# Performance work log

Measured on AMD Instinct MI355X. Metric: run time of the kernel, lower is better.

## Reference

```python
import jax, jax.numpy as jnp
import numpy as np
import math

# Static config (matches init_kwargs): C4 rotation group, 14x14 grid
B = 2
CIN = 96
MID = 96
HEADS = 8
COUT = 96
G = 4            # group elements (0/90/180/270 deg rotations)
S = 14           # spatial size == max_pos_embedding
HID = 16         # hidden width of the row/col embedding MLP (Conv2d 1->16)
DPOS = MID // 3                  # 32: row / col embedding dims
DG = MID - 2 * DPOS              # 32: group embedding dim


def setup_inputs() -> dict:
    key = jax.random.key(0)
    ks = jax.random.split(key, 12)

    def lin(k, shape, scale):
        return jax.random.normal(k, shape, jnp.float32) * scale

    x = jax.random.normal(ks[0], (B, CIN, G, S, S), jnp.float32)
    # 1x1x1 Conv3d weights == per-position linear layers [out, in]
    Wq = lin(ks[1], (MID * HEADS, CIN), 1.0 / np.sqrt(CIN)); bq = jnp.zeros((MID * HEADS,), jnp.float32)
    Wk = lin(ks[2], (MID * HEADS, CIN), 1.0 / np.sqrt(CIN)); bk = jnp.zeros((MID * HEADS,), jnp.float32)
    Wv = lin(ks[3], (MID * HEADS, CIN), 1.0 / np.sqrt(CIN)); bv = jnp.zeros((MID * HEADS,), jnp.float32)
    Wo = lin(ks[4], (COUT, MID * HEADS), 1.0 / np.sqrt(MID * HEADS)); bo = jnp.zeros((COUT,), jnp.float32)
    # row embedding MLP: scalar -> 16 -> LayerNorm -> Swish -> DPOS
    rw1 = lin(ks[5], (HID,), 1.0); rb1 = jnp.zeros((HID,), jnp.float32)
    rgam = jnp.ones((HID,), jnp.float32); rbet = jnp.zeros((HID,), jnp.float32)
    rw2 = lin(ks[6], (HID, DPOS), 1.0 / np.sqrt(HID)); rb2 = jnp.zeros((DPOS,), jnp.float32)
    # col embedding MLP
    cw1 = lin(ks[7], (HID,), 1.0); cb1 = jnp.zeros((HID,), jnp.float32)
    cgam = jnp.ones((HID,), jnp.float32); cbet = jnp.zeros((HID,), jnp.float32)
    cw2 = lin(ks[8], (HID, DPOS), 1.0 / np.sqrt(HID)); cb2 = jnp.zeros((DPOS,), jnp.float32)
    # group element embedding table
    gemb = lin(ks[9], (G, DG), 0.02)

    # Relative-position buffers: rel coordinate (k-i)/(S-1) in [-1,1], rotated by
    # each group element (left action of the rotation on R^2).  [G, S, S, S, S]
    d = (jnp.arange(S)[None, :] - jnp.arange(S)[:, None]).astype(jnp.float32) / (S - 1)
    dr = jnp.broadcast_to(d[:, None, :, None], (S, S, S, S))   # row offset (k-i)
    dc = jnp.broadcast_to(d[None, :, None, :], (S, S, S, S))   # col offset (l-j)
    ang = jnp.arange(G, dtype=jnp.float32) * (np.pi / 2.0)
    cs = jnp.cos(ang)[:, None, None, None, None]
    sn = jnp.sin(ang)[:, None, None, None, None]
    row_rel = cs * dr - sn * dc
    col_rel = sn * dr + cs * dc
    # relative group-element indices acted on by each group element v: [G, G, G]
    gi = jnp.arange(G)
    g_idx = (gi[None, None, :] - gi[None, :, None] + gi[:, None, None]) % G

    return {"x": x, "Wq": Wq, "bq": bq, "Wk": Wk, "bk": bk, "Wv": Wv, "bv": bv,
            "Wo": Wo, "bo": bo,
            "rw1": rw1, "rb1": rb1, "rgam": rgam, "rbet": rbet, "rw2": rw2, "rb2": rb2,
            "cw1": cw1, "cb1": cb1, "cgam": cgam, "cbet": cbet, "cw2": cw2, "cb2": cb2,
            "gemb": gemb, "row_rel": row_rel, "col_rel": col_rel, "g_idx": g_idx}


def _embed(rel, w1, b1, gam, bet, w2, b2):
    # Conv2d(1->16, k=1) + channel LayerNorm + Swish + Conv2d(16->DPOS, k=1)
    h = rel[..., None] * w1 + b1                                   # [..., 16]
    mu = jnp.mean(h, axis=-1, keepdims=True)
    var = jnp.var(h, axis=-1, keepdims=True)
    h = (h - mu) / jnp.sqrt(var + 1e-5) * gam + bet
    h = h * jax.nn.sigmoid(h)                                      # Swish
    return h @ w2 + b2                                             # [..., DPOS]


def reference(x, Wq, bq, Wk, bk, Wv, bv, Wo, bo,
              rw1, rb1, rgam, rbet, rw2, rb2,
              cw1, cb1, cgam, cbet, cw2, cb2,
              gemb, row_rel, col_rel, g_idx):
    b = x.shape[0]

    def proj(W, bias):
        y = jnp.einsum('bcgij,dc->bdgij', x, W) + bias[None, :, None, None, None]
        return y.reshape(b, MID, HEADS, G, S, S)   # split channels as (mid, heads)

    q = proj(Wq, bq)
    k = proj(Wk, bk)
    v = proj(Wv, bv)

    q_row = q[:, :DPOS]
    q_col = q[:, DPOS:2 * DPOS]
    q_grp = q[:, 2 * DPOS:]

    row_e = _embed(row_rel, rw1, rb1, rgam, rbet, rw2, rb2)        # [G,S,S,S,S,DPOS]
    col_e = _embed(col_rel, cw1, cb1, cgam, cbet, cw2, cb2)

    row_s = jnp.einsum('bchgij,vijklc->bhvgijkl', q_row, row_e)
    col_s = jnp.einsum('bchgij,vijklc->bhvgijkl', q_col, col_e)
    g_s = jnp.einsum('bchgij,vgmc->bhvgijm', q_grp, gemb[g_idx])
    content = jnp.einsum('bchgij,bchmkl->bhgijmkl', q, k)

    # broadcast add into [b, h, v, g, i, j, m, k, l]
    scores = (jnp.expand_dims(row_s + col_s, -3)
              + g_s[..., None, None]
              + content[:, :, None]) / math.sqrt(CIN)

    sh = scores.shape
    probs = jax.nn.softmax(scores.reshape(sh[:-3] + (-1,)), axis=-1).reshape(sh)

    vo = jnp.einsum('bhvgijmkl,bchmkl->bchvij', probs, v)
    vo = vo.reshape(b, MID * HEADS, G, S, S)
    return jnp.einsum('bcgij,dc->bdgij', vo, Wo) + bo[None, :, None, None, None]
```

## Files before the change

### kernel.cpp

```cpp
#include <hip/hip_runtime.h>
#include <hip/hip_bf16.h>

constexpr int kB   = 2;
constexpr int kH   = 8;
constexpr int kG   = 4;
constexpr int kS   = 14;
constexpr int kSS  = 196;
constexpr int kKey = 784;
constexpr int kKeyP = 800;
constexpr int kMid = 96;
constexpr int kQR  = 28;
constexpr int kPS  = 808;
constexpr int kTS  = 36;
constexpr float kScl = 0.10206207261596577f;
constexpr float kK2  = 0.14724663682f;
constexpr float kCc  = 11.5415603272f;

typedef __attribute__((ext_vector_type(8))) short bf16x8;
typedef __attribute__((ext_vector_type(4))) float f32x4;

constexpr size_t SZ_QKb = (size_t)kB*kH*kG*kSS*kMid/2;
constexpr size_t OFF_Qb = 0;
constexpr size_t OFF_Kb = OFF_Qb + SZ_QKb;
constexpr size_t OFF_V  = OFF_Kb + SZ_QKb;
constexpr size_t SZ_V   = (size_t)kB*kH*kMid*kKeyP/2;
constexpr size_t OFF_FR = OFF_V + SZ_V;
constexpr size_t OFF_FC = OFF_FR + 27*32;
constexpr size_t OFF_WOH = OFF_FC + 27*32;

__global__ __launch_bounds__(256)
void k_qkv(const float* __restrict__ x,
           const float* __restrict__ Wq, const float* __restrict__ bq,
           const float* __restrict__ Wk, const float* __restrict__ bk,
           const float* __restrict__ Wv, const float* __restrict__ bv,
           __hip_bfloat16* __restrict__ Qb, __hip_bfloat16* __restrict__ Kb,
           __hip_bfloat16* __restrict__ Vb,
           const float* __restrict__ rw1, const float* __restrict__ rb1,
           const float* __restrict__ rgam, const float* __restrict__ rbet,
           const float* __restrict__ rw2, const float* __restrict__ rb2,
           const float* __restrict__ cw1, const float* __restrict__ cb1,
           const float* __restrict__ cgam, const float* __restrict__ cbet,
           const float* __restrict__ cw2, const float* __restrict__ cb2,
           float* __restrict__ frow, float* __restrict__ fcol,
           const float* __restrict__ Wo, __hip_bfloat16* __restrict__ Woh,
           float* __restrict__ out0) {
  const int bid = blockIdx.x;
  const int ten = blockIdx.y;
  const int i = bid % 14;
  const int g = (bid / 14) % 4;
  const int b = bid / 56;
  const float* W    = (ten == 0) ? Wq : (ten == 1) ? Wk : Wv;
  const float* bias = (ten == 0) ? bq : (ten == 1) ? bk : bv;

  {
    int zidx = (ten*112 + bid)*256 + threadIdx.x;
    if (zidx < 37632) ((float4*)out0)[zidx] = make_float4(0.f, 0.f, 0.f, 0.f);
  }

  __shared__ alignas(16) float xs[14][100];
  for (int idx = threadIdx.x; idx < 96*14; idx += 256) {
    int cin = idx / 14, j = idx % 14;
    xs[j][cin] = x[((size_t)(b*96 + cin)*4 + g)*196 + i*14 + j];
  }
  __syncthreads();

  for (int d = threadIdx.x; d < 768; d += 256) {
    int c = d >> 3, h = d & 7;
    float bvv = bias[d];
    float acc[14];
#pragma unroll
    for (int j = 0; j < 14; ++j) acc[j] = bvv;
    const float* wrow = W + (size_t)d * 96;
    for (int cc = 0; cc < 96; cc += 4) {
      float4 w = *(const float4*)(wrow + cc);
#pragma unroll
      for (int j = 0; j < 14; ++j) {
        float4 xv = *(const float4*)(&xs[j][cc]);
        acc[j] += w.x*xv.x + w.y*xv.y + w.z*xv.z + w.w*xv.w;
      }
    }
    if (ten == 2) {
      __hip_bfloat16* op = Vb + ((size_t)((b*8 + h)*96 + c))*kKeyP + (i*14)*4 + g;
#pragma unroll
      for (int j = 0; j < 14; ++j) op[j*4] = __float2bfloat16(acc[j]);
    } else {
      __hip_bfloat16* dst = (ten == 0) ? Qb : Kb;
      __hip_bfloat16* op = dst + ((size_t)((b*8 + h)*4 + g)*196 + i*14)*96 + c;
#pragma unroll
      for (int j = 0; j < 14; ++j) op[(size_t)j*96] = __float2bfloat16(acc[j]);
    }
  }

  if (ten == 1) {
    for (int idx = bid*256 + threadIdx.x; idx < 73728; idx += 112*256) {
      int h = idx / 9216, rem = idx - h*9216;
      int d = rem / 96, c = rem - d*96;
      Woh[idx] = __float2bfloat16(Wo[(size_t)d*768 + c*8 + h]);
    }
  }
  if (ten == 2 && bid < 16) {
    for (int idx = threadIdx.x; idx < 96*16; idx += 256) {
      int c = idx >> 4, kp = idx & 15;
      Vb[((size_t)(bid*96 + c))*kKeyP + kKey + kp] = __float2bfloat16(0.f);
    }
  }
  if (ten == 0 && bid == 0 && threadIdx.x < 54) {
    int t = threadIdx.x;
    int which = t / 27;
    int n = t % 27;
    float tv = (float)(n - 13) / 13.0f;
    const float* w1  = which ? cw1  : rw1;
    const float* b1  = which ? cb1  : rb1;
    const float* gam = which ? cgam : rgam;
    const float* bet = which ? cbet : rbet;
    const float* w2  = which ? cw2  : rw2;
    const float* b2  = which ? cb2  : rb2;
    float h[16];
    float mu = 0.f;
#pragma unroll
    for (int d = 0; d < 16; ++d) { h[d] = tv * w1[d] + b1[d]; mu += h[d]; }
    mu *= (1.0f/16.0f);
    float var = 0.f;
#pragma unroll
    for (int d = 0; d < 16; ++d) { float z = h[d] - mu; var += z*z; }
    var *= (1.0f/16.0f);
    float rstd = rsqrtf(var + 1e-5f);
#pragma unroll
    for (int d = 0; d < 16; ++d) {
      float z = (h[d] - mu) * rstd * gam[d] + bet[d];
      h[d] = z / (1.0f + expf(-z));
    }
    float* outp = (which ? fcol : frow) + n*32;
    for (int c = 0; c < 32; ++c) {
      float o = b2[c];
#pragma unroll
      for (int d = 0; d < 16; ++d) o += h[d] * w2[d*32 + c];
      outp[c] = o;
    }
  }
}

__global__ __launch_bounds__(512, 4)
void k_attn(const __hip_bfloat16* __restrict__ Qb, const __hip_bfloat16* __restrict__ Kb,
            const float* __restrict__ frow_g, const float* __restrict__ fcol_g,
            const float* __restrict__ gemb_g,
            const __hip_bfloat16* __restrict__ Vb,
            const __hip_bfloat16* __restrict__ Woh,
            const float* __restrict__ bo, float* __restrict__ out) {
  const int tid = threadIdx.x;
  const int bid = blockIdx.x;
  const int jhalf = bid & 1;
  const int t2 = bid >> 1;
  const int qi = t2 % 14;
  const int hh = (t2 / 14) % 8;
  const int bb = t2 / 112;
  const int bh = bb*8 + hh;

  __shared__ alignas(16) char poolA[19104];
  __shared__ alignas(16) __hip_bfloat16 contl[kQR][kPS];
  __shared__ alignas(16) float ArrE[kQR][28];
  __shared__ alignas(16) float AclE[kQR][28];
  __shared__ alignas(16) float AgEall[4][kQR][4];
  __shared__ float T[4][kQR][14];
  __shared__ float DinvS[4][kQR];

  float (*qs)[96] = (float(*)[96])poolA;
  float* frowS = (float*)(poolA + 10752);
  float* fcolS = (float*)(poolA + 10752 + 3888);
  float* gembS = (float*)(poolA + 10752 + 2*3888);
  __hip_bfloat16 (*vos)[104] = (__hip_bfloat16(*)[104])poolA;

  const short* Qs = (const short*)Qb;
  const short* Ks = (const short*)Kb;

  for (int idx = tid; idx < kQR*96; idx += 512) {
    int q = idx / 96, c = idx - q*96;
    int g = q / 7, jq = q - g*7;
    qs[q][c] = __bfloat162float(
        Qb[((size_t)((bh*4 + g)*kSS + qi*14 + jhalf*7 + jq))*96 + c]);
  }
  for (int idx = tid; idx < 864; idx += 512) {
    int s = idx >> 5, c = idx & 31;
    frowS[s*kTS + c] = frow_g[idx] * kK2;
    fcolS[s*kTS + c] = fcol_g[idx] * kK2;
  }
  if (tid < 128) gembS[(tid >> 5)*kTS + (tid & 31)] = gemb_g[tid] * kK2;
  __syncthreads();

  for (int idx = tid; idx < kQR*24; idx += 512) {
    int r = idx / 24, c2 = idx - r*24;
    contl[r][784 + c2] = __float2bfloat16(0.f);
  }
  {
    const int lane = tid & 63;
    const int wave = tid >> 6;
    const int col  = lane & 15;
    const int quad = lane >> 4;

    bf16x8 afrag[2][3];
#pragma unroll
    for (int mt = 0; mt < 2; ++mt) {
      int m = mt*16 + col;
      int q = (m < kQR) ? m : 0;
      const short* qrow = Qs +
          ((size_t)((bh*4 + q/7)*kSS + qi*14 + jhalf*7 + q%7))*96;
#pragma unroll
      for (int ks = 0; ks < 3; ++ks)
        afrag[mt][ks] = *(const bf16x8*)(qrow + ks*32 + quad*8);
    }

    for (int nt = wave; nt < 49; nt += 8) {
      int kl = nt*16 + col;
      const short* krow = Ks + ((size_t)(bh*kKey + kl))*96;
      bf16x8 b0 = *(const bf16x8*)(krow + 0*32 + quad*8);
      bf16x8 b1 = *(const bf16x8*)(krow + 1*32 + quad*8);
      bf16x8 b2 = *(const bf16x8*)(krow + 2*32 + quad*8);
      f32x4 c0 = {0.f,0.f,0.f,0.f};
      f32x4 c1 = {0.f,0.f,0.f,0.f};
      c0 = __builtin_amdgcn_mfma_f32_16x16x32_bf16(afrag[0][0], b0, c0, 0, 0, 0);
      c0 = __builtin_amdgcn_mfma_f32_16x16x32_bf16(afrag[0][1], b1, c0, 0, 0, 0);
      c0 = __builtin_amdgcn_mfma_f32_16x16x32_bf16(afrag[0][2], b2, c0, 0, 0, 0);
      c1 = __builtin_amdgcn_mfma_f32_16x16x32_bf16(afrag[1][0], b0, c1, 0, 0, 0);
      c1 = __builtin_amdgcn_mfma_f32_16x16x32_bf16(afrag[1][1], b1, c1, 0, 0, 0);
      c1 = __builtin_amdgcn_mfma_f32_16x16x32_bf16(afrag[1][2], b2, c1, 0, 0, 0);
      int ijn = kl % 196, mk = kl / 196;
#pragma unroll
      for (int r = 0; r < 4; ++r) {
        int q0 = quad*4 + r;
        contl[q0][ijn*4 + mk] = __float2bfloat16(exp2f(c0[r]*kK2 - kCc));
        int q1 = 16 + quad*4 + r;
        if (q1 < kQR)
          contl[q1][ijn*4 + mk] = __float2bfloat16(exp2f(c1[r]*kK2 - kCc));
      }
    }
  }

  for (int t = tid; t < kQR*58; t += 512) {
    int q = t / 58, s = t - q*58;
    float acc = 0.f;
    if (s < 27) {
#pragma unroll
      for (int c = 0; c < 32; ++c) acc += qs[q][c] * frowS[s*kTS + c];
      ArrE[q][s] = exp2f(acc);
    } else if (s < 54) {
      int n = s - 27;
#pragma unroll
      for (int c = 0; c < 32; ++c) acc += qs[q][32+c] * fcolS[n*kTS + c];
      AclE[q][n] = exp2f(acc);
    } else {
      int p = s - 54;
#pragma unroll
      for (int c = 0; c < 32; ++c) acc += qs[q][64+c] * gembS[p*kTS + c];
      float e = exp2f(acc);
      int gq = q / 7;
#pragma unroll
      for (int vv = 0; vv < 4; ++vv)
        AgEall[vv][q][(p + gq - vv + 8) & 3] = e;
    }
  }
  __syncthreads();

  const int actv = (tid < 392);
  const int qB  = actv ? (tid / 14) : 0;
  const int kkB = actv ? (tid % 14) : 0;
  const int jlB = jhalf*7 + (qB % 7);
  const int daB = kkB - qi;
  const int half = actv ? (tid / 196) : 0;
  const int ijC  = actv ? (tid % 196) : 0;
  const int kkC = ijC / 14;
  const int llC = ijC % 14;
  const int daC = kkC - qi;

  if (actv) {
    f32x4 ag0 = *(const f32x4*)(&AgEall[0][qB][0]);
    f32x4 ag1 = *(const f32x4*)(&AgEall[1][qB][0]);
    f32x4 ag2 = *(const f32x4*)(&AgEall[2][qB][0]);
    f32x4 ag3 = *(const f32x4*)(&AgEall[3][qB][0]);
    const float* Ar = &ArrE[qB][13];
    const float* Ac = &AclE[qB][13];
    float a0 = 0.f, a1 = 0.f, a2 = 0.f, a3 = 0.f;
#pragma unroll
    for (int ll = 0; ll < 14; ++ll) {
      const int db = ll - jlB;
      ushort4 u = *(const ushort4*)(&contl[qB][(kkB*14 + ll)*4]);
      float e0 = __uint_as_float((unsigned)u.x << 16);
      float e1 = __uint_as_float((unsigned)u.y << 16);
      float e2 = __uint_as_float((unsigned)u.z << 16);
      float e3 = __uint_as_float((unsigned)u.w << 16);
      a0 += Ac[ db] * (e0*ag0.x + e1*ag0.y + e2*ag0.z + e3*ag0.w);
      a1 += Ar[-db] * (e0*ag1.x + e1*ag1.y + e2*ag1.z + e3*ag1.w);
      a2 += Ac[-db] * (e0*ag2.x + e1*ag2.y + e2*ag2.z + e3*ag2.w);
      a3 += Ar[ db] * (e0*ag3.x + e1*ag3.y + e2*ag3.z + e3*ag3.w);
    }
    T[0][qB][kkB] = Ar[ daB] * a0;
    T[1][qB][kkB] = Ac[ daB] * a1;
    T[2][qB][kkB] = Ar[-daB] * a2;
    T[3][qB][kkB] = Ac[-daB] * a3;
  }
  __syncthreads();
  if (tid < 112) {
    int v = tid / 28, q = tid - v*28;
    float dsum = 0.f;
#pragma unroll
    for (int kk = 0; kk < 14; ++kk) dsum += T[v][q][kk];
    DinvS[v][q] = 1.0f / dsum;
  }
  __syncthreads();

  if (actv) {
    unsigned p32[kQR];
#pragma unroll
    for (int q = 0; q < kQR; ++q)
      p32[q] = *(const unsigned*)(&contl[q][ijC*4 + half*2]);
#pragma unroll
    for (int v = 0; v < 4; ++v) {
      const int s1a = (v==0) ? 1 : (v==2) ? -1 : 0;
      const int s1b = (v==1) ? -1 : (v==3) ? 1 : 0;
      const int s2a = (v==1) ? 1 : (v==3) ? -1 : 0;
      const int s2b = (v==0) ? 1 : (v==2) ? -1 : 0;
#pragma unroll
      for (int jq = 0; jq < 7; ++jq) {
        const int db = llC - (jhalf*7 + jq);
        const int ai = s1a*daC + s1b*db, ci = s2a*daC + s2b*db;
        float am0 = 0.f, am1 = 0.f;
#pragma unroll
        for (int gq = 0; gq < 4; ++gq) {
          const int q = gq*7 + jq;
          const float fq = ArrE[q][13 + ai] * AclE[q][13 + ci] * DinvS[v][q];
          unsigned u = p32[q];
          float e0 = __uint_as_float(u << 16);
          float e1 = __uint_as_float(u & 0xffff0000u);
          am0 += e0 * (AgEall[v][q][half*2]     * fq);
          am1 += e1 * (AgEall[v][q][half*2 + 1] * fq);
        }
        __hip_bfloat16* pp = &contl[jq*4 + v][ijC*4 + half*2];
        pp[0] = __float2bfloat16(am0);
        pp[1] = __float2bfloat16(am1);
      }
    }
  }
  __syncthreads();

  const int lane = tid & 63;
  const int wave = tid >> 6;
  const int col  = lane & 15;
  const int quad = lane >> 4;
  const int b_ = bh >> 3, h_ = bh & 7;

  {
    const short* Bp = (const short*)Vb + ((size_t)bh*96)*kKeyP + quad*8;
#pragma unroll
    for (int tk = 0; tk < 2; ++tk) {
      int t = wave + tk*8;
      if (t < 12) {
        int mt = t / 6, nt = t - mt*6;
        int crow = nt*16 + col;
        int prow = mt*16 + col; if (prow >= kQR) prow = 0;
        const short* ap = (const short*)(&contl[prow][0]) + quad*8;
        const short* bp = Bp + (size_t)crow*kKeyP;
        f32x4 acc = {0.f,0.f,0.f,0.f};
        for (int ks = 0; ks < 25; ++ks) {
          bf16x8 a = *(const bf16x8*)(ap + ks*32);
          bf16x8 b = *(const bf16x8*)(bp + ks*32);
          acc = __builtin_amdgcn_mfma_f32_16x16x32_bf16(a, b, acc, 0, 0, 0);
        }
#pragma unroll
        for (int r = 0; r < 4; ++r)
          vos[mt*16 + quad*4 + r][crow] = __float2bfloat16(acc[r]);
      }
    }
  }
  __syncthreads();

  {
    const short* wb = (const short*)Woh + (size_t)h_*9216;
#pragma unroll
    for (int tk = 0; tk < 2; ++tk) {
      int t = wave + tk*8;
      if (t < 12) {
        int mt = t / 6, dt = t - mt*6;
        f32x4 acc = {0.f,0.f,0.f,0.f};
#pragma unroll
        for (int ks = 0; ks < 3; ++ks) {
          bf16x8 a = *(const bf16x8*)(&vos[mt*16 + col][ks*32 + quad*8]);
          bf16x8 b = *(const bf16x8*)(wb + (size_t)(dt*16 + col)*96 + ks*32 + quad*8);
          acc = __builtin_amdgcn_mfma_f32_16x16x32_bf16(a, b, acc, 0, 0, 0);
        }
        const int d = dt*16 + col;
        const float bias = (h_ == 0) ? bo[d] : 0.f;
#pragma unroll
        for (int r = 0; r < 4; ++r) {
          int rr = mt*16 + quad*4 + r;
          if (rr < kQR) {
            int jq = rr >> 2, vv = rr & 3;
            int ijq = qi*14 + jhalf*7 + jq;
            atomicAdd(&out[((size_t)(b_*96 + d)*4 + vv)*kSS + ijq], acc[r] + bias);
          }
        }
      }
    }
  }
}

extern "C" void kernel_launch(void* const* d_in, const int* in_sizes, int n_in,
                              void* d_out, int out_size, void* d_ws, size_t ws_size,
                              hipStream_t stream) {
  const float* x    = (const float*)d_in[0];
  const float* Wq   = (const float*)d_in[1];
  const float* bq   = (const float*)d_in[2];
  const float* Wk   = (const float*)d_in[3];
  const float* bk   = (const float*)d_in[4];
  const float* Wv   = (const float*)d_in[5];
  const float* bv   = (const float*)d_in[6];
  const float* Wo   = (const float*)d_in[7];
  const float* bo   = (const float*)d_in[8];
  const float* rw1  = (const float*)d_in[9];
  const float* rb1  = (const float*)d_in[10];
  const float* rgam = (const float*)d_in[11];
  const float* rbet = (const float*)d_in[12];
  const float* rw2  = (const float*)d_in[13];
  const float* rb2  = (const float*)d_in[14];
  const float* cw1  = (const float*)d_in[15];
  const float* cb1  = (const float*)d_in[16];
  const float* cgam = (const float*)d_in[17];
  const float* cbet = (const float*)d_in[18];
  const float* cw2  = (const float*)d_in[19];
  const float* cb2  = (const float*)d_in[20];
  const float* gemb = (const float*)d_in[21];

  float* ws = (float*)d_ws;
  __hip_bfloat16* Qb = (__hip_bfloat16*)(ws + OFF_Qb);
  __hip_bfloat16* Kb = (__hip_bfloat16*)(ws + OFF_Kb);
  __hip_bfloat16* Vb = (__hip_bfloat16*)(ws + OFF_V);
  float* Frow = ws + OFF_FR;
  float* Fcol = ws + OFF_FC;
  __hip_bfloat16* Woh = (__hip_bfloat16*)(ws + OFF_WOH);
  float* out  = (float*)d_out;

  k_qkv<<<dim3(112, 3), 256, 0, stream>>>(x, Wq, bq, Wk, bk, Wv, bv, Qb, Kb, Vb,
                                          rw1, rb1, rgam, rbet, rw2, rb2,
                                          cw1, cb1, cgam, cbet, cw2, cb2,
                                          Frow, Fcol, Wo, Woh, out);
  k_attn<<<448, 512, 0, stream>>>(Qb, Kb, Frow, Fcol, gemb, Vb, Woh, bo, out);
}
```

Measured before the change: 189.8 us.

## Compute QKV projection with bf16 MFMA tiles instead of scalar FP32 loops

Rewrites the QKV projection kernel so each block stages a bf16 copy of the input slice (all 196 positions for one batch/group) and a 128-row weight tile in shared memory. Each wave then computes 16x16 output tiles with three bf16 MFMA instructions. The grid drops from 112x3 blocks of 256 threads to 48x3 blocks of 512 threads. The goal is to replace slow FP32 scalar FMA loops with matrix cores, at the cost of rounding x and the weights to bf16 before accumulation and of scattered 2-byte output stores.

After: 165.7 us. 1.15x faster.

```diff
diff --git a/kernel.cpp b/kernel.cpp
--- a/kernel.cpp
+++ b/kernel.cpp
@@ -12,6 +12,7 @@
 constexpr int kQR  = 28;
 constexpr int kPS  = 808;
 constexpr int kTS  = 36;
+constexpr int kXS  = 104;
 constexpr float kScl = 0.10206207261596577f;
 constexpr float kK2  = 0.14724663682f;
 constexpr float kCc  = 11.5415603272f;
@@ -28,7 +29,7 @@
 constexpr size_t OFF_FC = OFF_FR + 27*32;
 constexpr size_t OFF_WOH = OFF_FC + 27*32;
 
-__global__ __launch_bounds__(256)
+__global__ __launch_bounds__(512, 4)
 void k_qkv(const float* __restrict__ x,
            const float* __restrict__ Wq, const float* __restrict__ bq,
            const float* __restrict__ Wk, const float* __restrict__ bk,
@@ -46,66 +47,102 @@
            float* __restrict__ out0) {
   const int bid = blockIdx.x;
   const int ten = blockIdx.y;
-  const int i = bid % 14;
-  const int g = (bid / 14) % 4;
-  const int b = bid / 56;
+  const int tid = threadIdx.x;
+  const int mc = bid % 6;
+  const int g  = (bid / 6) % 4;
+  const int b  = bid / 24;
+  const int d0 = mc * 128;
   const float* W    = (ten == 0) ? Wq : (ten == 1) ? Wk : Wv;
   const float* bias = (ten == 0) ? bq : (ten == 1) ? bk : bv;
 
   {
-    int zidx = (ten*112 + bid)*256 + threadIdx.x;
+    int zidx = (ten*48 + bid)*512 + tid;
     if (zidx < 37632) ((float4*)out0)[zidx] = make_float4(0.f, 0.f, 0.f, 0.f);
   }
 
-  __shared__ alignas(16) float xs[14][100];
-  for (int idx = threadIdx.x; idx < 96*14; idx += 256) {
-    int cin = idx / 14, j = idx % 14;
-    xs[j][cin] = x[((size_t)(b*96 + cin)*4 + g)*196 + i*14 + j];
-  }
-  __syncthreads();
-
-  for (int d = threadIdx.x; d < 768; d += 256) {
-    int c = d >> 3, h = d & 7;
-    float bvv = bias[d];
-    float acc[14];
-#pragma unroll
-    for (int j = 0; j < 14; ++j) acc[j] = bvv;
-    const float* wrow = W + (size_t)d * 96;
-    for (int cc = 0; cc < 96; cc += 4) {
-      float4 w = *(const float4*)(wrow + cc);
-#pragma unroll
-      for (int j = 0; j < 14; ++j) {
-        float4 xv = *(const float4*)(&xs[j][cc]);
-        acc[j] += w.x*xv.x + w.y*xv.y + w.z*xv.z + w.w*xv.w;
+  __shared__ alignas(16) __hip_bfloat16 Xt[208][kXS];
+  __shared__ alignas(16) __hip_bfloat16 Ws[128][kXS];
+
+  for (int idx = tid; idx < 24*208; idx += 512) {
+    int cq = idx / 208, ij = idx - cq*208;
+    float4 v = make_float4(0.f, 0.f, 0.f, 0.f);
+    if (ij < 196) {
+      const float* xp = x + (((size_t)b*96 + cq*4)*4 + (size_t)g)*196 + ij;
+      v.x = xp[0]; v.y = xp[784]; v.z = xp[1568]; v.w = xp[2352];
+    }
+    ushort4 u;
+    u.x = __bfloat16_as_ushort(__float2bfloat16(v.x));
+    u.y = __bfloat16_as_ushort(__float2bfloat16(v.y));
+    u.z = __bfloat16_as_ushort(__float2bfloat16(v.z));
+    u.w = __bfloat16_as_ushort(__float2bfloat16(v.w));
+    *(ushort4*)(&Xt[ij][cq*4]) = u;
+  }
+  for (int idx = tid; idx < 128*24; idx += 512) {
+    int dl = idx / 24, cq = idx - dl*24;
+    float4 v = *(const float4*)(W + (size_t)(d0 + dl)*96 + cq*4);
+    ushort4 u;
+    u.x = __bfloat16_as_ushort(__float2bfloat16(v.x));
+    u.y = __bfloat16_as_ushort(__float2bfloat16(v.y));
+    u.z = __bfloat16_as_ushort(__float2bfloat16(v.z));
+    u.w = __bfloat16_as_ushort(__float2bfloat16(v.w));
+    *(ushort4*)(&Ws[dl][cq*4]) = u;
+  }
+  __syncthreads();
+
+  {
+    const int lane = tid & 63;
+    const int wave = tid >> 6;
+    const int col  = lane & 15;
+    const int quad = lane >> 4;
+    const short* ar = (const short*)(&Ws[wave*16 + col][0]);
+    bf16x8 a0 = *(const bf16x8*)(ar + 0*32 + quad*8);
+    bf16x8 a1 = *(const bf16x8*)(ar + 1*32 + quad*8);
+    bf16x8 a2 = *(const bf16x8*)(ar + 2*32 + quad*8);
+    float4 b4 = *(const float4*)(bias + d0 + wave*16 + quad*4);
+    float bb[4] = {b4.x, b4.y, b4.z, b4.w};
+
+    for (int nt = 0; nt < 13; ++nt) {
+      const short* xr = (const short*)(&Xt[nt*16 + col][0]);
+      bf16x8 x0 = *(const bf16x8*)(xr + 0*32 + quad*8);
+      bf16x8 x1 = *(const bf16x8*)(xr + 1*32 + quad*8);
+      bf16x8 x2 = *(const bf16x8*)(xr + 2*32 + quad*8);
+      f32x4 acc = {0.f, 0.f, 0.f, 0.f};
+      acc = __builtin_amdgcn_mfma_f32_16x16x32_bf16(a0, x0, acc, 0, 0, 0);
+      acc = __builtin_amdgcn_mfma_f32_16x16x32_bf16(a1, x1, acc, 0, 0, 0);
+      acc = __builtin_amdgcn_mfma_f32_16x16x32_bf16(a2, x2, acc, 0, 0, 0);
+      int ij = nt*16 + col;
+      if (ij < 196) {
+#pragma unroll
+        for (int r = 0; r < 4; ++r) {
+          int d = d0 + wave*16 + quad*4 + r;
+          int c = d >> 3, h = d & 7;
+          float val = acc[r] + bb[r];
+          if (ten == 2) {
+            Vb[((size_t)((b*8 + h)*96 + c))*kKeyP + ij*4 + g] = __float2bfloat16(val);
+          } else {
+            __hip_bfloat16* dst = (ten == 0) ? Qb : Kb;
+            dst[((size_t)((b*8 + h)*4 + g)*196 + ij)*96 + c] = __float2bfloat16(val);
+          }
+        }
       }
     }
-    if (ten == 2) {
-      __hip_bfloat16* op = Vb + ((size_t)((b*8 + h)*96 + c))*kKeyP + (i*14)*4 + g;
-#pragma unroll
-      for (int j = 0; j < 14; ++j) op[j*4] = __float2bfloat16(acc[j]);
-    } else {
-      __hip_bfloat16* dst = (ten == 0) ? Qb : Kb;
-      __hip_bfloat16* op = dst + ((size_t)((b*8 + h)*4 + g)*196 + i*14)*96 + c;
-#pragma unroll
-      for (int j = 0; j < 14; ++j) op[(size_t)j*96] = __float2bfloat16(acc[j]);
-    }
   }
 
   if (ten == 1) {
-    for (int idx = bid*256 + threadIdx.x; idx < 73728; idx += 112*256) {
+    for (int idx = bid*512 + tid; idx < 73728; idx += 48*512) {
       int h = idx / 9216, rem = idx - h*9216;
       int d = rem / 96, c = rem - d*96;
       Woh[idx] = __float2bfloat16(Wo[(size_t)d*768 + c*8 + h]);
     }
   }
   if (ten == 2 && bid < 16) {
-    for (int idx = threadIdx.x; idx < 96*16; idx += 256) {
+    for (int idx = tid; idx < 96*16; idx += 512) {
       int c = idx >> 4, kp = idx & 15;
       Vb[((size_t)(bid*96 + c))*kKeyP + kKey + kp] = __float2bfloat16(0.f);
     }
   }
-  if (ten == 0 && bid == 0 && threadIdx.x < 54) {
-    int t = threadIdx.x;
+  if (ten == 0 && bid == 0 && tid < 54) {
+    int t = tid;
     int which = t / 27;
     int n = t % 27;
     float tv = (float)(n - 13) / 13.0f;
@@ -437,9 +474,9 @@
   __hip_bfloat16* Woh = (__hip_bfloat16*)(ws + OFF_WOH);
   float* out  = (float*)d_out;
 
-  k_qkv<<<dim3(112, 3), 256, 0, stream>>>(x, Wq, bq, Wk, bk, Wv, bv, Qb, Kb, Vb,
-                                          rw1, rb1, rgam, rbet, rw2, rb2,
-                                          cw1, cb1, cgam, cbet, cw2, cb2,
-                                          Frow, Fcol, Wo, Woh, out);
+  k_qkv<<<dim3(48, 3), 512, 0, stream>>>(x, Wq, bq, Wk, bk, Wv, bv, Qb, Kb, Vb,
+                                         rw1, rb1, rgam, rbet, rw2, rb2,
+                                         cw1, cb1, cgam, cbet, cw2, cb2,
+                                         Frow, Fcol, Wo, Woh, out);
   k_attn<<<448, 512, 0, stream>>>(Qb, Kb, Frow, Fcol, gemb, Vb, Woh, bo, out);
 }
```
